# Performance work log

Hardware: AMD Instinct MI355X
Metric: run time of the kernel (lower is better)

The kernel has to match this reference:

```python
import jax, jax.numpy as jnp
import numpy as np

N_NODES = 100000
N_EDGES = 1000000
EMB = 64
HID = 64
N_CLASSES = 1
LEAKY_SLOPE = 0.01  # flax.linen.leaky_relu default


def setup_inputs() -> dict:
    key = jax.random.key(0)
    k1, k2, k3, k4, k5 = jax.random.split(key, 5)
    node_ids = jnp.arange(N_NODES, dtype=jnp.int32)
    senders = jax.random.randint(k1, (N_EDGES,), 0, N_NODES, dtype=jnp.int32)
    receivers = jax.random.randint(k2, (N_EDGES,), 0, N_NODES, dtype=jnp.int32)
    embed_table = jax.random.normal(k3, (N_NODES, EMB), dtype=jnp.float32) * 0.05
    W1 = jax.random.normal(k4, (EMB, HID), dtype=jnp.float32) * (1.0 / np.sqrt(EMB))
    W2 = jax.random.normal(k5, (HID, N_CLASSES), dtype=jnp.float32) * (1.0 / np.sqrt(HID))
    b2 = jnp.zeros((N_CLASSES,), dtype=jnp.float32)
    return {"node_ids": node_ids, "senders": senders, "receivers": receivers,
            "embed_table": embed_table, "W1": W1, "W2": W2, "b2": b2}


def gcn_aggregate(x, senders, receivers, n_nodes, symmetric):
    # Faithful to jraph.GraphConvolution: update_node_fn is applied BEFORE this.
    if symmetric:
        ones = jnp.ones_like(senders, dtype=x.dtype)
        send_deg = jax.ops.segment_sum(ones, senders, num_segments=n_nodes)
        recv_deg = jax.ops.segment_sum(ones, receivers, num_segments=n_nodes)
        x = x * jax.lax.rsqrt(jnp.maximum(send_deg, 1.0))[:, None]
        x = jax.ops.segment_sum(x[senders], receivers, num_segments=n_nodes)  # [N, d]
        x = x * jax.lax.rsqrt(jnp.maximum(recv_deg, 1.0))[:, None]
    else:
        x = jax.ops.segment_sum(x[senders], receivers, num_segments=n_nodes)
    return x


def reference(node_ids, senders, receivers, embed_table, W1, W2, b2):
    n = node_ids.shape[0]
    # GraphMapFeatures(embed_node_fn=nn.Embed(...))
    x = embed_table[node_ids]                      # [N, EMB]
    # GraphConvolution(Dense(hidden, use_bias=False), symmetric_normalization=True)
    x = x @ W1                                     # [N, HID]
    x = gcn_aggregate(x, senders, receivers, n, symmetric=True)
    x = jax.nn.leaky_relu(x, negative_slope=LEAKY_SLOPE)
    # GraphConvolution(Dense(classes), symmetric_normalization=False)
    x = x @ W2 + b2                                # [N, C]
    x = gcn_aggregate(x, senders, receivers, n, symmetric=False)
    return jax.nn.sigmoid(x)
```

## Files before the change

kernel.cpp:

```cpp
#include <hip/hip_runtime.h>
#include <hip/hip_bf16.h>

#define N_NODES 100000
#define N_EDGES 1000000
#define SCAN_B 256
#define N_BLOCKS_SCAN ((N_NODES + SCAN_B - 1) / SCAN_B)
#define H_BLOCKS 1024

#define RANGES 4
#define RSIZE  25000
#define RWORDS 12500
#define CHUNKS 32
#define CHUNK_EDGES (N_EDGES / CHUNKS)
#define HRSIZE  12500
#define HRWORDS 6250


__device__ __forceinline__ unsigned f32_to_bf16(float v) {
    unsigned u = __float_as_uint(v);
    return (u + 0x7fffu + ((u >> 16) & 1u)) >> 16;
}

__global__ void k_hist(const int* __restrict__ senders,
                       const int* __restrict__ receivers,
                       unsigned* __restrict__ ghist_s,
                       unsigned* __restrict__ ghist_r) {
    __shared__ unsigned lds[RWORDS];
    int blk = blockIdx.x;
    int arr = blk >> 7;
    int rem = blk & 127;
    int r   = rem >> 5;
    int c   = rem & 31;
    const int* __restrict__ src = arr ? receivers : senders;
    unsigned* __restrict__ gh   = arr ? ghist_r : ghist_s;
    int t = threadIdx.x;

    for (int w = t; w < RWORDS; w += 1024) lds[w] = 0u;
    __syncthreads();

    int base = r * RSIZE;
    int beg  = c * CHUNK_EDGES;
    int end  = beg + CHUNK_EDGES;
    for (int i = beg + t; i < end; i += 1024) {
        unsigned idx = (unsigned)(src[i] - base);
        if (idx < (unsigned)RSIZE)
            atomicAdd(&lds[idx >> 1], 1u << ((idx & 1) * 16));
    }
    __syncthreads();

    unsigned* __restrict__ dst = gh + (size_t)rem * RWORDS;
    for (int w = t; w < RWORDS; w += 1024) dst[w] = lds[w];
}

__global__ void k_scanA2(const unsigned* __restrict__ ghist_s,
                         const unsigned* __restrict__ ghist_r,
                         int* __restrict__ cnt_r, float* __restrict__ rs,
                         int* __restrict__ blockSums) {
    __shared__ int s[SCAN_B];
    int t = threadIdx.x;
    int idx = blockIdx.x * SCAN_B + t;
    int v = 0;
    if (idx < N_NODES) {
        int r = idx / RSIZE;
        int bin = idx - r * RSIZE;
        int w = bin >> 1, sh = (bin & 1) * 16;
        const unsigned* __restrict__ gr = ghist_r + (size_t)(r * CHUNKS) * RWORDS + w;
        const unsigned* __restrict__ gs = ghist_s + (size_t)(r * CHUNKS) * RWORDS + w;
        unsigned sr_ = 0, ss_ = 0;
#pragma unroll
        for (int c = 0; c < CHUNKS; ++c) {
            sr_ += (gr[(size_t)c * RWORDS] >> sh) & 0xffffu;
            ss_ += (gs[(size_t)c * RWORDS] >> sh) & 0xffffu;
        }
        v = (int)sr_;
        cnt_r[idx] = v;
        rs[idx] = rsqrtf(fmaxf((float)ss_, 1.0f));
    }
    s[t] = v;
    __syncthreads();
    for (int off = 1; off < SCAN_B; off <<= 1) {
        int x = (t >= off) ? s[t - off] : 0;
        __syncthreads();
        s[t] += x;
        __syncthreads();
    }
    if (t == SCAN_B - 1) blockSums[blockIdx.x] = s[t];
}

__global__ void k_scanCD_h(const int* __restrict__ cnt_r,
                           const int* __restrict__ blockSums,
                           const unsigned* __restrict__ ghist_r,
                           int* __restrict__ row_start,
                           int* __restrict__ coff,
                           const float* __restrict__ emb,
                           const float* __restrict__ rs,
                           const float* __restrict__ W1,
                           unsigned short* __restrict__ h16) {
    __shared__ int s[SCAN_B];
    int t = threadIdx.x;
    int b = blockIdx.x;

    if (b < N_BLOCKS_SCAN) {
        int acc = 0;
        for (int j = t; j < b; j += SCAN_B) acc += blockSums[j];
        s[t] = acc;
        __syncthreads();
        for (int off = SCAN_B / 2; off > 0; off >>= 1) {
            if (t < off) s[t] += s[t + off];
            __syncthreads();
        }
        int blockOff = s[0];
        __syncthreads();

        int idx = b * SCAN_B + t;
        int v = (idx < N_NODES) ? cnt_r[idx] : 0;
        s[t] = v;
        __syncthreads();
        for (int off = 1; off < SCAN_B; off <<= 1) {
            int x = (t >= off) ? s[t - off] : 0;
            __syncthreads();
            s[t] += x;
            __syncthreads();
        }
        if (idx < N_NODES) {
            int run = blockOff + s[t] - v;
            row_start[idx] = run;
            int r = idx / RSIZE;
            int bin = idx - r * RSIZE;
            int w = bin >> 1, sh = (bin & 1) * 16;
            const unsigned* __restrict__ gr = ghist_r + (size_t)(r * CHUNKS) * RWORDS + w;
            int* __restrict__ co = coff + (size_t)(r * CHUNKS) * RSIZE + bin;
#pragma unroll
            for (int c = 0; c < CHUNKS; ++c) {
                co[(size_t)c * RSIZE] = run;
                run += (int)((gr[(size_t)c * RWORDS] >> sh) & 0xffffu);
            }
        }
        if (b == 0 && t == 0) row_start[N_NODES] = N_EDGES;
    } else {
        int lane = t & 63;
        int wib  = t >> 6;
        int gw   = (b - N_BLOCKS_SCAN) * 4 + wib;
        const int nw = H_BLOCKS * 4;

        float w1c[64];
#pragma unroll
        for (int k = 0; k < 64; ++k) w1c[k] = W1[k * 64 + lane];

        for (int n = gw; n < N_NODES; n += nw) {
            float e = emb[(size_t)n * 64 + lane] * rs[n];
            float a = 0.f;
            int ei = __float_as_int(e);
#pragma unroll
            for (int k = 0; k < 64; ++k)
                a += __int_as_float(__builtin_amdgcn_readlane(ei, k)) * w1c[k];
            h16[(size_t)n * 64 + lane] = (unsigned short)f32_to_bf16(a);
        }
    }
}

__global__ void k_fill2(const int* __restrict__ senders,
                        const int* __restrict__ receivers,
                        const int* __restrict__ coff,
                        int* __restrict__ col) {
    __shared__ unsigned lds[HRWORDS];
    int r8 = blockIdx.x >> 5;
    int c  = blockIdx.x & 31;
    int sr = r8 >> 1, hs = r8 & 1;
    int t  = threadIdx.x;

    for (int w = t; w < HRWORDS; w += 1024) lds[w] = 0u;
    __syncthreads();

    int base = r8 * HRSIZE;
    int beg  = c * CHUNK_EDGES, end = beg + CHUNK_EDGES;
    const int* __restrict__ co =
        coff + (size_t)(sr * CHUNKS + c) * RSIZE + hs * HRSIZE;
    for (int i = beg + t; i < end; i += 1024) {
        unsigned idx = (unsigned)(receivers[i] - base);
        if (idx < (unsigned)HRSIZE) {
            int sh = (idx & 1) * 16;
            unsigned old = atomicAdd(&lds[idx >> 1], 1u << sh);
            int rank = (int)((old >> sh) & 0xffffu);
            col[co[idx] + rank] = senders[i];
        }
    }
}

__global__ void k_agg_post(const int* __restrict__ row_start,
                           const int* __restrict__ col,
                           const unsigned* __restrict__ h32,
                           const float* __restrict__ W2,
                           const float* __restrict__ b2,
                           float* __restrict__ z) {
    int gtid = blockIdx.x * blockDim.x + threadIdx.x;
    int wid  = gtid >> 6;
    int lane = threadIdx.x & 63;
    int half = lane >> 5;
    int hl   = lane & 31;
    int n = wid * 2 + half;
    if (n >= N_NODES) return;

    int start = row_start[n];
    int end   = row_start[n + 1];
    float a0 = 0.f, a1 = 0.f;
    int i = start;
    for (; i + 3 < end; i += 4) {
        int s0 = col[i], s1 = col[i + 1], s2 = col[i + 2], s3 = col[i + 3];
        unsigned u0 = h32[(size_t)s0 * 32 + hl];
        unsigned u1 = h32[(size_t)s1 * 32 + hl];
        unsigned u2 = h32[(size_t)s2 * 32 + hl];
        unsigned u3 = h32[(size_t)s3 * 32 + hl];
        a0 += (__uint_as_float(u0 << 16) + __uint_as_float(u1 << 16)) +
              (__uint_as_float(u2 << 16) + __uint_as_float(u3 << 16));
        a1 += (__uint_as_float(u0 & 0xffff0000u) + __uint_as_float(u1 & 0xffff0000u)) +
              (__uint_as_float(u2 & 0xffff0000u) + __uint_as_float(u3 & 0xffff0000u));
    }
    for (; i < end; ++i) {
        unsigned u = h32[(size_t)col[i] * 32 + hl];
        a0 += __uint_as_float(u << 16);
        a1 += __uint_as_float(u & 0xffff0000u);
    }

    float rsq = rsqrtf(fmaxf((float)(end - start), 1.0f));
    float x0 = a0 * rsq, x1 = a1 * rsq;
    x0 = (x0 > 0.f) ? x0 : 0.01f * x0;
    x1 = (x1 > 0.f) ? x1 : 0.01f * x1;
    float2 w2 = ((const float2*)W2)[hl];
    float p = x0 * w2.x + x1 * w2.y;
#pragma unroll
    for (int off = 16; off > 0; off >>= 1) p += __shfl_xor(p, off, 64);
    if (hl == 0) z[n] = p + b2[0];
}

__global__ void k_agg2_sigmoid(const int* __restrict__ row_start,
                               const int* __restrict__ col,
                               const float* __restrict__ z,
                               float* __restrict__ out) {
    int n = blockIdx.x * blockDim.x + threadIdx.x;
    if (n >= N_NODES) return;
    int start = row_start[n];
    int end   = row_start[n + 1];
    float acc = 0.f;
    int i = start;
    for (; i + 3 < end; i += 4) {
        float a = z[col[i]],     b = z[col[i + 1]];
        float c = z[col[i + 2]], d = z[col[i + 3]];
        acc += (a + b) + (c + d);
    }
    for (; i < end; ++i) acc += z[col[i]];
    out[n] = 1.0f / (1.0f + expf(-acc));
}

extern "C" void kernel_launch(void* const* d_in, const int* in_sizes, int n_in,
                              void* d_out, int out_size, void* d_ws, size_t ws_size,
                              hipStream_t stream) {
    const int* senders    = (const int*)d_in[1];
    const int* receivers  = (const int*)d_in[2];
    const float* emb      = (const float*)d_in[3];
    const float* W1       = (const float*)d_in[4];
    const float* W2       = (const float*)d_in[5];
    const float* b2       = (const float*)d_in[6];
    float* out            = (float*)d_out;

    char* ws = (char*)d_ws;
    unsigned*       ghist_s   = (unsigned*)(ws);
    unsigned*       ghist_r   = (unsigned*)(ws + 6400000);
    int*            coff      = (int*)(ws + 12800000);
    int*            cnt_r     = (int*)(ws + 25600000);
    int*            row_start = (int*)(ws + 26000000);
    int*            blockSums = (int*)(ws + 26400016);
    float*          rs        = (float*)(ws + 26403200);
    int*            col       = (int*)(ws + 26803200);
    unsigned short* h16       = (unsigned short*)(ws + 30803200);
    float*          z         = (float*)(ws + 43603200);

    const int B = 256;
    k_hist<<<2 * RANGES * CHUNKS, 1024, 0, stream>>>(senders, receivers, ghist_s, ghist_r);
    k_scanA2<<<N_BLOCKS_SCAN, SCAN_B, 0, stream>>>(ghist_s, ghist_r, cnt_r, rs, blockSums);
    k_scanCD_h<<<N_BLOCKS_SCAN + H_BLOCKS, B, 0, stream>>>(
        cnt_r, blockSums, ghist_r, row_start, coff, emb, rs, W1, h16);
    k_fill2<<<RANGES * CHUNKS * 2, 1024, 0, stream>>>(senders, receivers, coff, col);
    k_agg_post<<<12500, B, 0, stream>>>(row_start, col, (const unsigned*)h16, W2, b2, z);
    k_agg2_sigmoid<<<(N_NODES + B - 1) / B, B, 0, stream>>>(row_start, col, z, out);
}
```

Measured before the change: 212.1 us.

## Record per-edge ranks during histogram and make CSR fill a flat scatter

```diff
diff --git a/kernel.cpp b/kernel.cpp
--- a/kernel.cpp
+++ b/kernel.cpp
@@ -12,8 +12,6 @@
 #define RWORDS 12500
 #define CHUNKS 32
 #define CHUNK_EDGES (N_EDGES / CHUNKS)
-#define HRSIZE  12500
-#define HRWORDS 6250
 
 
 __device__ __forceinline__ unsigned f32_to_bf16(float v) {
@@ -24,7 +22,8 @@
 __global__ void k_hist(const int* __restrict__ senders,
                        const int* __restrict__ receivers,
                        unsigned* __restrict__ ghist_s,
-                       unsigned* __restrict__ ghist_r) {
+                       unsigned* __restrict__ ghist_r,
+                       unsigned short* __restrict__ rank16) {
     __shared__ unsigned lds[RWORDS];
     int blk = blockIdx.x;
     int arr = blk >> 7;
@@ -43,8 +42,11 @@
     int end  = beg + CHUNK_EDGES;
     for (int i = beg + t; i < end; i += 1024) {
         unsigned idx = (unsigned)(src[i] - base);
-        if (idx < (unsigned)RSIZE)
-            atomicAdd(&lds[idx >> 1], 1u << ((idx & 1) * 16));
+        if (idx < (unsigned)RSIZE) {
+            int sh = (idx & 1) * 16;
+            unsigned old = atomicAdd(&lds[idx >> 1], 1u << sh);
+            if (arr) rank16[i] = (unsigned short)((old >> sh) & 0xffffu);
+        }
     }
     __syncthreads();
 
@@ -162,29 +164,16 @@
 __global__ void k_fill2(const int* __restrict__ senders,
                         const int* __restrict__ receivers,
                         const int* __restrict__ coff,
+                        const unsigned short* __restrict__ rank16,
                         int* __restrict__ col) {
-    __shared__ unsigned lds[HRWORDS];
-    int r8 = blockIdx.x >> 5;
-    int c  = blockIdx.x & 31;
-    int sr = r8 >> 1, hs = r8 & 1;
-    int t  = threadIdx.x;
-
-    for (int w = t; w < HRWORDS; w += 1024) lds[w] = 0u;
-    __syncthreads();
-
-    int base = r8 * HRSIZE;
-    int beg  = c * CHUNK_EDGES, end = beg + CHUNK_EDGES;
-    const int* __restrict__ co =
-        coff + (size_t)(sr * CHUNKS + c) * RSIZE + hs * HRSIZE;
-    for (int i = beg + t; i < end; i += 1024) {
-        unsigned idx = (unsigned)(receivers[i] - base);
-        if (idx < (unsigned)HRSIZE) {
-            int sh = (idx & 1) * 16;
-            unsigned old = atomicAdd(&lds[idx >> 1], 1u << sh);
-            int rank = (int)((old >> sh) & 0xffffu);
-            col[co[idx] + rank] = senders[i];
-        }
-    }
+    int i = blockIdx.x * blockDim.x + threadIdx.x;
+    if (i >= N_EDGES) return;
+    int rv = receivers[i];
+    int r  = rv / RSIZE;
+    int bin = rv - r * RSIZE;
+    int c  = i / CHUNK_EDGES;
+    int co = coff[(size_t)(r * CHUNKS + c) * RSIZE + bin];
+    col[co + (int)rank16[i]] = senders[i];
 }
 
 __global__ void k_agg_post(const int* __restrict__ row_start,
@@ -274,13 +263,14 @@
     int*            col       = (int*)(ws + 26803200);
     unsigned short* h16       = (unsigned short*)(ws + 30803200);
     float*          z         = (float*)(ws + 43603200);
+    unsigned short* rank16    = (unsigned short*)(ws + 44003200);
 
     const int B = 256;
-    k_hist<<<2 * RANGES * CHUNKS, 1024, 0, stream>>>(senders, receivers, ghist_s, ghist_r);
+    k_hist<<<2 * RANGES * CHUNKS, 1024, 0, stream>>>(senders, receivers, ghist_s, ghist_r, rank16);
     k_scanA2<<<N_BLOCKS_SCAN, SCAN_B, 0, stream>>>(ghist_s, ghist_r, cnt_r, rs, blockSums);
     k_scanCD_h<<<N_BLOCKS_SCAN + H_BLOCKS, B, 0, stream>>>(
         cnt_r, blockSums, ghist_r, row_start, coff, emb, rs, W1, h16);
-    k_fill2<<<RANGES * CHUNKS * 2, 1024, 0, stream>>>(senders, receivers, coff, col);
+    k_fill2<<<(N_EDGES + B - 1) / B, B, 0, stream>>>(senders, receivers, coff, rank16, col);
     k_agg_post<<<12500, B, 0, stream>>>(row_start, col, (const unsigned*)h16, W2, b2, z);
     k_agg2_sigmoid<<<(N_NODES + B - 1) / B, B, 0, stream>>>(row_start, col, z, out);
 }
```

Result: no change. 213.9 us (+0.9%).

## Fuse both aggregation kernels into one cooperative kernel with grid sync

Applied to the files above, without the earlier changes.

```diff
diff --git a/kernel.cpp b/kernel.cpp
--- a/kernel.cpp
+++ b/kernel.cpp
@@ -1,11 +1,15 @@
 #include <hip/hip_runtime.h>
 #include <hip/hip_bf16.h>
+#include <hip/hip_cooperative_groups.h>
+
+namespace cg = cooperative_groups;
 
 #define N_NODES 100000
 #define N_EDGES 1000000
 #define SCAN_B 256
 #define N_BLOCKS_SCAN ((N_NODES + SCAN_B - 1) / SCAN_B)
 #define H_BLOCKS 1024
+#define AGG_BLOCKS 1024
 
 #define RANGES 4
 #define RSIZE  25000
@@ -187,69 +191,74 @@
     }
 }
 
-__global__ void k_agg_post(const int* __restrict__ row_start,
-                           const int* __restrict__ col,
-                           const unsigned* __restrict__ h32,
-                           const float* __restrict__ W2,
-                           const float* __restrict__ b2,
-                           float* __restrict__ z) {
-    int gtid = blockIdx.x * blockDim.x + threadIdx.x;
-    int wid  = gtid >> 6;
+__global__ void __launch_bounds__(256)
+k_agg_both(const int* __restrict__ row_start,
+           const int* __restrict__ col,
+           const unsigned* __restrict__ h32,
+           const float* __restrict__ W2,
+           const float* __restrict__ b2,
+           float* __restrict__ z,
+           float* __restrict__ out) {
+    cg::grid_group grid = cg::this_grid();
     int lane = threadIdx.x & 63;
+    int wib  = threadIdx.x >> 6;
+    int gw   = blockIdx.x * 4 + wib;
+    const int nw = AGG_BLOCKS * 4;
     int half = lane >> 5;
     int hl   = lane & 31;
-    int n = wid * 2 + half;
-    if (n >= N_NODES) return;
-
-    int start = row_start[n];
-    int end   = row_start[n + 1];
-    float a0 = 0.f, a1 = 0.f;
-    int i = start;
-    for (; i + 3 < end; i += 4) {
-        int s0 = col[i], s1 = col[i + 1], s2 = col[i + 2], s3 = col[i + 3];
-        unsigned u0 = h32[(size_t)s0 * 32 + hl];
-        unsigned u1 = h32[(size_t)s1 * 32 + hl];
-        unsigned u2 = h32[(size_t)s2 * 32 + hl];
-        unsigned u3 = h32[(size_t)s3 * 32 + hl];
-        a0 += (__uint_as_float(u0 << 16) + __uint_as_float(u1 << 16)) +
-              (__uint_as_float(u2 << 16) + __uint_as_float(u3 << 16));
-        a1 += (__uint_as_float(u0 & 0xffff0000u) + __uint_as_float(u1 & 0xffff0000u)) +
-              (__uint_as_float(u2 & 0xffff0000u) + __uint_as_float(u3 & 0xffff0000u));
-    }
-    for (; i < end; ++i) {
-        unsigned u = h32[(size_t)col[i] * 32 + hl];
-        a0 += __uint_as_float(u << 16);
-        a1 += __uint_as_float(u & 0xffff0000u);
-    }
-
-    float rsq = rsqrtf(fmaxf((float)(end - start), 1.0f));
-    float x0 = a0 * rsq, x1 = a1 * rsq;
-    x0 = (x0 > 0.f) ? x0 : 0.01f * x0;
-    x1 = (x1 > 0.f) ? x1 : 0.01f * x1;
     float2 w2 = ((const float2*)W2)[hl];
-    float p = x0 * w2.x + x1 * w2.y;
-#pragma unroll
-    for (int off = 16; off > 0; off >>= 1) p += __shfl_xor(p, off, 64);
-    if (hl == 0) z[n] = p + b2[0];
-}
-
-__global__ void k_agg2_sigmoid(const int* __restrict__ row_start,
-                               const int* __restrict__ col,
-                               const float* __restrict__ z,
-                               float* __restrict__ out) {
-    int n = blockIdx.x * blockDim.x + threadIdx.x;
-    if (n >= N_NODES) return;
-    int start = row_start[n];
-    int end   = row_start[n + 1];
-    float acc = 0.f;
-    int i = start;
-    for (; i + 3 < end; i += 4) {
-        float a = z[col[i]],     b = z[col[i + 1]];
-        float c = z[col[i + 2]], d = z[col[i + 3]];
-        acc += (a + b) + (c + d);
-    }
-    for (; i < end; ++i) acc += z[col[i]];
-    out[n] = 1.0f / (1.0f + expf(-acc));
+    float bias = b2[0];
+
+    for (int wid = gw; wid < N_NODES / 2; wid += nw) {
+        int n = wid * 2 + half;
+        int start = row_start[n];
+        int end   = row_start[n + 1];
+        float a0 = 0.f, a1 = 0.f;
+        int i = start;
+        for (; i + 3 < end; i += 4) {
+            int s0 = col[i], s1 = col[i + 1], s2 = col[i + 2], s3 = col[i + 3];
+            unsigned u0 = h32[(size_t)s0 * 32 + hl];
+            unsigned u1 = h32[(size_t)s1 * 32 + hl];
+            unsigned u2 = h32[(size_t)s2 * 32 + hl];
+            unsigned u3 = h32[(size_t)s3 * 32 + hl];
+            a0 += (__uint_as_float(u0 << 16) + __uint_as_float(u1 << 16)) +
+                  (__uint_as_float(u2 << 16) + __uint_as_float(u3 << 16));
+            a1 += (__uint_as_float(u0 & 0xffff0000u) + __uint_as_float(u1 & 0xffff0000u)) +
+                  (__uint_as_float(u2 & 0xffff0000u) + __uint_as_float(u3 & 0xffff0000u));
+        }
+        for (; i < end; ++i) {
+            unsigned u = h32[(size_t)col[i] * 32 + hl];
+            a0 += __uint_as_float(u << 16);
+            a1 += __uint_as_float(u & 0xffff0000u);
+        }
+
+        float rsq = rsqrtf(fmaxf((float)(end - start), 1.0f));
+        float x0 = a0 * rsq, x1 = a1 * rsq;
+        x0 = (x0 > 0.f) ? x0 : 0.01f * x0;
+        x1 = (x1 > 0.f) ? x1 : 0.01f * x1;
+        float p = x0 * w2.x + x1 * w2.y;
+#pragma unroll
+        for (int off = 16; off > 0; off >>= 1) p += __shfl_xor(p, off, 64);
+        if (hl == 0) z[n] = p + bias;
+    }
+
+    grid.sync();
+
+    int tid = blockIdx.x * blockDim.x + threadIdx.x;
+    const int nt = AGG_BLOCKS * 256;
+    for (int n = tid; n < N_NODES; n += nt) {
+        int start = row_start[n];
+        int end   = row_start[n + 1];
+        float acc = 0.f;
+        int i = start;
+        for (; i + 3 < end; i += 4) {
+            float a = z[col[i]],     b = z[col[i + 1]];
+            float c = z[col[i + 2]], d = z[col[i + 3]];
+            acc += (a + b) + (c + d);
+        }
+        for (; i < end; ++i) acc += z[col[i]];
+        out[n] = 1.0f / (1.0f + expf(-acc));
+    }
 }
 
 extern "C" void kernel_launch(void* const* d_in, const int* in_sizes, int n_in,
@@ -281,6 +290,12 @@
     k_scanCD_h<<<N_BLOCKS_SCAN + H_BLOCKS, B, 0, stream>>>(
         cnt_r, blockSums, ghist_r, row_start, coff, emb, rs, W1, h16);
     k_fill2<<<RANGES * CHUNKS * 2, 1024, 0, stream>>>(senders, receivers, coff, col);
-    k_agg_post<<<12500, B, 0, stream>>>(row_start, col, (const unsigned*)h16, W2, b2, z);
-    k_agg2_sigmoid<<<(N_NODES + B - 1) / B, B, 0, stream>>>(row_start, col, z, out);
-}
+
+    const unsigned* h32 = (const unsigned*)h16;
+    void* args[] = {
+        (void*)&row_start, (void*)&col, (void*)&h32,
+        (void*)&W2, (void*)&b2, (void*)&z, (void*)&out
+    };
+    hipLaunchCooperativeKernel((const void*)k_agg_both, dim3(AGG_BLOCKS), dim3(B),
+                               args, 0, stream);
+}
```

New measurement: 377.4 us. 1.78x slower.
